# Kernel tuning notes

Hardware: AMD Instinct MI355X
Metric: run time of the kernel (lower is better)

## Reference

```python
import jax, jax.numpy as jnp
import numpy as np

B, S, H = 32, 2048, 1024
UNITS = 1024


def setup_inputs() -> dict:
    key = jax.random.key(0)
    ks = jax.random.split(key, 8)
    scale_h = 1.0 / np.sqrt(H)
    scale_u = 1.0 / np.sqrt(UNITS)
    return {
        "query": jax.random.normal(ks[0], (B, H), dtype=jnp.float32),
        "values": jax.random.normal(ks[1], (B, S, H), dtype=jnp.float32),
        "W1": jax.random.normal(ks[2], (H, UNITS), dtype=jnp.float32) * scale_h,
        "b1": jnp.zeros((UNITS,), dtype=jnp.float32),
        "W2": jax.random.normal(ks[3], (H, UNITS), dtype=jnp.float32) * scale_h,
        "b2": jnp.zeros((UNITS,), dtype=jnp.float32),
        "V": jax.random.normal(ks[4], (UNITS, 1), dtype=jnp.float32) * scale_u,
        "bv": jnp.zeros((1,), dtype=jnp.float32),
    }


def reference(query, values, W1, b1, W2, b2, V, bv):
    # proj_v: [B, S, units]; proj_q: [B, 1, units] (query expanded on time axis)
    proj_v = jnp.einsum("bsh,hu->bsu", values, W1) + b1
    proj_q = (query @ W2 + b2)[:, None, :]
    # score: [B, S, 1]
    score = jnp.tanh(proj_v + proj_q) @ V + bv
    attention_weights = jax.nn.softmax(score, axis=1)  # softmax over seq axis
    context_vector = jnp.sum(attention_weights * values, axis=1)  # [B, H]
    return context_vector, attention_weights
```

## Files before the change

kernel.cpp:

```cpp
#include <hip/hip_runtime.h>

#define H 1024
#define UNITS 1024
#define BATCH 32
#define SEQ 2048
#define M_TOT (BATCH * SEQ)

typedef __attribute__((ext_vector_type(8))) short bf16x8;
typedef __attribute__((ext_vector_type(8))) unsigned short u16x8;
typedef __attribute__((ext_vector_type(4))) float f32x4;

__device__ __forceinline__ unsigned short f2bf(float f) {
  union { float f; unsigned u; } x; x.f = f;
  unsigned r = x.u + 0x7FFFu + ((x.u >> 16) & 1u);
  return (unsigned short)(r >> 16);
}
__device__ __forceinline__ float bf2f(unsigned short h) {
  union { unsigned u; float f; } x; x.u = (unsigned)h << 16;
  return x.f;
}

__device__ __forceinline__ void gll16(const unsigned short* g, unsigned short* l) {
  __builtin_amdgcn_global_load_lds(
      (const __attribute__((address_space(1))) void*)g,
      (__attribute__((address_space(3))) void*)l, 16, 0, 0);
}

__global__ void k_cast(const float* __restrict__ in, unsigned short* __restrict__ out) {
  size_t i = ((size_t)blockIdx.x * 256 + threadIdx.x) * 8;
  float4 v0 = *reinterpret_cast<const float4*>(in + i);
  float4 v1 = *reinterpret_cast<const float4*>(in + i + 4);
  union { unsigned short h[8]; u16x8 v; } p;
  p.h[0] = f2bf(v0.x); p.h[1] = f2bf(v0.y); p.h[2] = f2bf(v0.z); p.h[3] = f2bf(v0.w);
  p.h[4] = f2bf(v1.x); p.h[5] = f2bf(v1.y); p.h[6] = f2bf(v1.z); p.h[7] = f2bf(v1.w);
  *reinterpret_cast<u16x8*>(out + i) = p.v;
}

__global__ void k_transpose_w1(const float* __restrict__ W1, unsigned short* __restrict__ W1T) {
  __shared__ float tile[32][33];
  int bx = blockIdx.x, by = blockIdx.y;
  int tx = threadIdx.x, ty = threadIdx.y;
#pragma unroll
  for (int i = 0; i < 4; ++i)
    tile[ty + i * 8][tx] = W1[(by * 32 + ty + i * 8) * UNITS + bx * 32 + tx];
  __syncthreads();
#pragma unroll
  for (int i = 0; i < 4; ++i)
    W1T[(bx * 32 + ty + i * 8) * H + by * 32 + tx] = f2bf(tile[tx][ty + i * 8]);
}

__global__ void k_projq(const float* __restrict__ query, const float* __restrict__ W2,
                        const float* __restrict__ b2, float* __restrict__ projq) {
  __shared__ float q[H];
  int b = blockIdx.x;
  int u = blockIdx.y * 256 + threadIdx.x;
  for (int i = threadIdx.x; i < H; i += 256) q[i] = query[b * H + i];
  __syncthreads();
  float acc = 0.f;
#pragma unroll 8
  for (int k = 0; k < H; ++k) acc = fmaf(q[k], W2[k * UNITS + u], acc);
  projq[b * UNITS + u] = acc + b2[u];
}

#define BM 256
#define BN 256
#define NKT 32

__global__ __launch_bounds__(512, 2) void k_score3(
    const unsigned short* __restrict__ Vb,
    const unsigned short* __restrict__ W1T,
    const float* __restrict__ b1,
    const float* __restrict__ projq,
    const float* __restrict__ V,
    float* __restrict__ scores)
{
  __shared__ unsigned short As[4][128][64];
  __shared__ unsigned short Bs[4][128][64];

  const int tid = threadIdx.x;
  const int lane = tid & 63;
  const int wave = tid >> 6;
  const int wm = wave >> 2;
  const int wn = wave & 3;
  const int li = lane & 15, hi = lane >> 4;
  const int lr2 = li >> 1;
  const int pcol = (((((li & 1) << 2) + hi) ^ lr2) & 7) << 3;

  const int g = blockIdx.x;
  const int xcd = g & 7;
  const int local = g >> 3;
  const int n_t = local & 3;
  const int m_t = xcd + ((local >> 2) << 3);
  const int m0 = m_t * BM;
  const int n0 = n_t * BN;

  const int sL = (lane & 7) ^ (lane >> 3);
  const int srow = 2 * (lane >> 3) + (sL >> 2);
  const int scol = (sL & 3) << 3;

  auto STAGE_A = [&](int bf, int kt) {
#pragma unroll
    for (int q = 0; q < 2; ++q) {
      int mb = wave * 32 + q * 16;
      gll16(&Vb[(size_t)(m0 + mb + srow) * H + kt * 32 + scol],
            &As[bf][wave * 16 + q * 8][0]);
    }
  };
  auto STAGE_B = [&](int bf, int kt) {
#pragma unroll
    for (int q = 0; q < 2; ++q) {
      int mb = wave * 32 + q * 16;
      gll16(&W1T[(size_t)(n0 + mb + srow) * H + kt * 32 + scol],
            &Bs[bf][wave * 16 + q * 8][0]);
    }
  };

  f32x4 acc[8][4] = {};

  STAGE_A(0, 0); STAGE_B(0, 0);
  STAGE_A(1, 1); STAGE_B(1, 1);
  STAGE_A(2, 2); STAGE_B(2, 2);
  asm volatile("s_waitcnt vmcnt(8)" ::: "memory");
  __builtin_amdgcn_s_barrier();

#pragma unroll 4
  for (int c = 0; c < NKT; ++c) {
    const int buf = c & 3;
    const int nbuf = (c + 3) & 3;
    const int cn = (c < NKT - 3) ? c + 3 : NKT - 1;

    bf16x8 a0[4], a1[4], b[4];

#pragma unroll
    for (int i = 0; i < 4; ++i)
      a0[i] = *reinterpret_cast<const bf16x8*>(&As[buf][wm * 64 + i * 8 + lr2][pcol]);
#pragma unroll
    for (int j = 0; j < 4; ++j)
      b[j] = *reinterpret_cast<const bf16x8*>(&Bs[buf][wn * 32 + j * 8 + lr2][pcol]);
    STAGE_A(nbuf, cn);
    __builtin_amdgcn_s_barrier();
    asm volatile("s_waitcnt lgkmcnt(0)" ::: "memory");
    __builtin_amdgcn_sched_barrier(0);
    __builtin_amdgcn_s_setprio(1);
#pragma unroll
    for (int i = 0; i < 4; ++i)
#pragma unroll
      for (int j = 0; j < 4; ++j)
        acc[i][j] = __builtin_amdgcn_mfma_f32_16x16x32_bf16(a0[i], b[j], acc[i][j], 0, 0, 0);
    __builtin_amdgcn_s_setprio(0);
    __builtin_amdgcn_s_barrier();

#pragma unroll
    for (int i = 0; i < 4; ++i)
      a1[i] = *reinterpret_cast<const bf16x8*>(&As[buf][wm * 64 + (i + 4) * 8 + lr2][pcol]);
    STAGE_B(nbuf, cn);
    asm volatile("s_waitcnt vmcnt(8)" ::: "memory");
    __builtin_amdgcn_s_barrier();
    asm volatile("s_waitcnt lgkmcnt(0)" ::: "memory");
    __builtin_amdgcn_sched_barrier(0);
    __builtin_amdgcn_s_setprio(1);
#pragma unroll
    for (int i = 0; i < 4; ++i)
#pragma unroll
      for (int j = 0; j < 4; ++j)
        acc[i + 4][j] = __builtin_amdgcn_mfma_f32_16x16x32_bf16(a1[i], b[j], acc[i + 4][j], 0, 0, 0);
    __builtin_amdgcn_s_setprio(0);
    __builtin_amdgcn_s_barrier();
  }

  const int b = m0 >> 11;
  float bias[4], vv[4];
#pragma unroll
  for (int j = 0; j < 4; ++j) {
    int u = n0 + wn * 64 + j * 16 + li;
    bias[j] = b1[u] + projq[b * UNITS + u];
    vv[j] = V[u];
  }
#pragma unroll
  for (int mi = 0; mi < 8; ++mi) {
#pragma unroll
    for (int r = 0; r < 4; ++r) {
      float s = 0.f;
#pragma unroll
      for (int j = 0; j < 4; ++j) {
        float x = acc[mi][j][r] + bias[j];
        float e = __expf(2.f * x);
        s += (1.f - 2.f / (e + 1.f)) * vv[j];
      }
      s += __shfl_xor(s, 1);
      s += __shfl_xor(s, 2);
      s += __shfl_xor(s, 4);
      s += __shfl_xor(s, 8);
      if (li == 0) {
        int row = m0 + wm * 128 + mi * 16 + hi * 4 + r;
        atomicAdd(&scores[row], s);
      }
    }
  }
}

#define FBM 128
#define FBN 128
#define FBK 64
#define LDK 72
__global__ __launch_bounds__(256) void k_score_f32(
    const float* __restrict__ values, const unsigned short* __restrict__ W1T,
    const float* __restrict__ b1, const float* __restrict__ projq,
    const float* __restrict__ V, float* __restrict__ scores)
{
  __shared__ unsigned short Asf[FBM][LDK];
  __shared__ unsigned short Bsf[FBN][LDK];
  const int tid = threadIdx.x;
  const int lane = tid & 63;
  const int wave = tid >> 6;
  const int wm = wave >> 1, wn = wave & 1;
  const int li = lane & 15, hi = lane >> 4;
  const int n0 = blockIdx.x * FBN;
  const int m0 = blockIdx.y * FBM;
  f32x4 acc[4][4] = {};
  for (int k0 = 0; k0 < H; k0 += FBK) {
    __syncthreads();
#pragma unroll
    for (int q = 0; q < 8; ++q) {
      int idx = q * 256 + tid;
      int row = idx >> 4;
      int kc = (idx & 15) << 2;
      float4 v = *reinterpret_cast<const float4*>(&values[(size_t)(m0 + row) * H + k0 + kc]);
      union { unsigned short h[4]; unsigned long long u64; } p;
      p.h[0] = f2bf(v.x); p.h[1] = f2bf(v.y); p.h[2] = f2bf(v.z); p.h[3] = f2bf(v.w);
      *reinterpret_cast<unsigned long long*>(&Asf[row][kc]) = p.u64;
    }
#pragma unroll
    for (int q = 0; q < 4; ++q) {
      int idx = q * 256 + tid;
      int row = idx >> 3;
      int kc = (idx & 7) << 3;
      *reinterpret_cast<u16x8*>(&Bsf[row][kc]) =
          *reinterpret_cast<const u16x8*>(&W1T[(size_t)(n0 + row) * H + k0 + kc]);
    }
    __syncthreads();
#pragma unroll
    for (int ks = 0; ks < 2; ++ks) {
      const int kofs = ks * 32 + 8 * hi;
      bf16x8 a[4], bb[4];
#pragma unroll
      for (int i = 0; i < 4; ++i)
        a[i] = *reinterpret_cast<const bf16x8*>(&Asf[wm * 64 + i * 16 + li][kofs]);
#pragma unroll
      for (int i = 0; i < 4; ++i)
        bb[i] = *reinterpret_cast<const bf16x8*>(&Bsf[wn * 64 + i * 16 + li][kofs]);
#pragma unroll
      for (int mi = 0; mi < 4; ++mi)
#pragma unroll
        for (int ni = 0; ni < 4; ++ni)
          acc[mi][ni] = __builtin_amdgcn_mfma_f32_16x16x32_bf16(a[mi], bb[ni], acc[mi][ni], 0, 0, 0);
    }
  }
  const int b = m0 >> 11;
  float bias[4], vv[4];
#pragma unroll
  for (int ni = 0; ni < 4; ++ni) {
    int u = n0 + wn * 64 + ni * 16 + li;
    bias[ni] = b1[u] + projq[b * UNITS + u];
    vv[ni] = V[u];
  }
#pragma unroll
  for (int mi = 0; mi < 4; ++mi) {
#pragma unroll
    for (int r = 0; r < 4; ++r) {
      float s = 0.f;
#pragma unroll
      for (int ni = 0; ni < 4; ++ni) {
        float x = acc[mi][ni][r] + bias[ni];
        float e = __expf(2.f * x);
        s += (1.f - 2.f / (e + 1.f)) * vv[ni];
      }
      s += __shfl_xor(s, 1);
      s += __shfl_xor(s, 2);
      s += __shfl_xor(s, 4);
      s += __shfl_xor(s, 8);
      if (li == 0) atomicAdd(&scores[m0 + wm * 64 + mi * 16 + hi * 4 + r], s);
    }
  }
}

__global__ void k_softmax(const float* __restrict__ scores, float* __restrict__ wts) {
  __shared__ float red[8];
  int b = blockIdx.x;
  int t = threadIdx.x;
  float v[8];
  float mx = -3.4e38f;
#pragma unroll
  for (int i = 0; i < 8; ++i) {
    v[i] = scores[b * SEQ + i * 256 + t];
    mx = fmaxf(mx, v[i]);
  }
#pragma unroll
  for (int o = 1; o < 64; o <<= 1) mx = fmaxf(mx, __shfl_xor(mx, o));
  if ((t & 63) == 0) red[t >> 6] = mx;
  __syncthreads();
  mx = fmaxf(fmaxf(red[0], red[1]), fmaxf(red[2], red[3]));
  float sum = 0.f;
#pragma unroll
  for (int i = 0; i < 8; ++i) { v[i] = __expf(v[i] - mx); sum += v[i]; }
#pragma unroll
  for (int o = 1; o < 64; o <<= 1) sum += __shfl_xor(sum, o);
  if ((t & 63) == 0) red[4 + (t >> 6)] = sum;
  __syncthreads();
  float inv = 1.f / (red[4] + red[5] + red[6] + red[7]);
#pragma unroll
  for (int i = 0; i < 8; ++i) wts[b * SEQ + i * 256 + t] = v[i] * inv;
}

__global__ void k_context_bf(const unsigned short* __restrict__ Vb,
                             const float* __restrict__ wts, float* __restrict__ ctx) {
  int b = blockIdx.x, sc = blockIdx.y;
  int h4 = threadIdx.x * 4;
  const unsigned short* vb = Vb + (size_t)b * SEQ * H;
  float a0 = 0, a1 = 0, a2 = 0, a3 = 0;
  int s0 = sc * 128;
#pragma unroll 4
  for (int s = s0; s < s0 + 128; ++s) {
    float w = wts[b * SEQ + s];
    ushort4 v = *reinterpret_cast<const ushort4*>(&vb[(size_t)s * H + h4]);
    a0 = fmaf(w, bf2f(v.x), a0);
    a1 = fmaf(w, bf2f(v.y), a1);
    a2 = fmaf(w, bf2f(v.z), a2);
    a3 = fmaf(w, bf2f(v.w), a3);
  }
  atomicAdd(&ctx[b * H + h4 + 0], a0);
  atomicAdd(&ctx[b * H + h4 + 1], a1);
  atomicAdd(&ctx[b * H + h4 + 2], a2);
  atomicAdd(&ctx[b * H + h4 + 3], a3);
}

__global__ void k_context(const float* __restrict__ values, const float* __restrict__ wts,
                          float* __restrict__ ctx) {
  int b = blockIdx.x, hc = blockIdx.y, sc = blockIdx.z;
  int h = hc * 256 + threadIdx.x;
  const float* vb = values + (size_t)b * SEQ * H;
  float acc = 0.f;
  int s0 = sc * 128;
#pragma unroll 4
  for (int s = s0; s < s0 + 128; ++s)
    acc = fmaf(wts[b * SEQ + s], vb[(size_t)s * H + h], acc);
  atomicAdd(&ctx[b * H + h], acc);
}

extern "C" void kernel_launch(void* const* d_in, const int* in_sizes, int n_in,
                              void* d_out, int out_size, void* d_ws, size_t ws_size,
                              hipStream_t stream) {
  (void)in_sizes; (void)n_in; (void)out_size;
  const float* query  = (const float*)d_in[0];
  const float* values = (const float*)d_in[1];
  const float* W1     = (const float*)d_in[2];
  const float* b1     = (const float*)d_in[3];
  const float* W2     = (const float*)d_in[4];
  const float* b2     = (const float*)d_in[5];
  const float* V      = (const float*)d_in[6];

  float* out = (float*)d_out;
  float* ctx = out;
  float* wts = out + BATCH * H;

  const size_t vb_bytes = (size_t)M_TOT * H * 2;
  const size_t need = vb_bytes + (2u << 20) + (256u << 10) + (128u << 10);

  if (ws_size >= need) {
    char* ws = (char*)d_ws;
    unsigned short* Vb  = (unsigned short*)ws;
    unsigned short* W1T = (unsigned short*)(ws + vb_bytes);
    float* scores = (float*)(ws + vb_bytes + (2u << 20));
    float* projq  = (float*)(ws + vb_bytes + (2u << 20) + (256u << 10));

    hipMemsetAsync(scores, 0, M_TOT * sizeof(float), stream);
    hipMemsetAsync(ctx, 0, BATCH * H * sizeof(float), stream);

    k_cast<<<(M_TOT * H / 8) / 256, 256, 0, stream>>>(values, Vb);
    k_transpose_w1<<<dim3(32, 32), dim3(32, 8), 0, stream>>>(W1, W1T);
    k_projq<<<dim3(32, 4), 256, 0, stream>>>(query, W2, b2, projq);
    k_score3<<<(M_TOT / BM) * (UNITS / BN), 512, 0, stream>>>(Vb, W1T, b1, projq, V, scores);
    k_softmax<<<BATCH, 256, 0, stream>>>(scores, wts);
    k_context_bf<<<dim3(BATCH, 16), 256, 0, stream>>>(Vb, wts, ctx);
  } else {
    char* ws = (char*)d_ws;
    unsigned short* W1T = (unsigned short*)ws;
    float* scores = (float*)(ws + (2u << 20));
    float* projq  = (float*)(ws + (2u << 20) + (256u << 10));

    hipMemsetAsync(scores, 0, M_TOT * sizeof(float), stream);
    hipMemsetAsync(ctx, 0, BATCH * H * sizeof(float), stream);

    k_transpose_w1<<<dim3(32, 32), dim3(32, 8), 0, stream>>>(W1, W1T);
    k_projq<<<dim3(32, 4), 256, 0, stream>>>(query, W2, b2, projq);
    k_score_f32<<<dim3(UNITS / FBN, M_TOT / FBM), 256, 0, stream>>>(values, W1T, b1, projq, V, scores);
    k_softmax<<<BATCH, 256, 0, stream>>>(scores, wts);
    k_context<<<dim3(BATCH, H / 256, 16), 256, 0, stream>>>(values, wts, ctx);
  }
}
```

Before: 335.3 us.

## Software-pipeline LDS fragment reads with MFMA in GEMM main loop

Restructures the K-loop so the LDS reads for the next half-tile and next tile are issued before the current MFMAs, using double-buffered B fragment registers and partial lgkmcnt waits instead of full lgkmcnt(0) drains. Barriers per tile drop from four to one. The aim is to hide LDS read latency behind matrix work and cut synchronization overhead. It raises register pressure and depends on fine-grained waitcnt counts being correct, so miscounting could cause races.

```diff
diff --git a/kernel.cpp b/kernel.cpp
--- a/kernel.cpp
+++ b/kernel.cpp
@@ -116,57 +116,80 @@
   };
 
   f32x4 acc[8][4] = {};
+  bf16x8 aH0[4], aH1[4], bX[4], bY[4];
+
+  auto READ_H0 = [&](int t, bf16x8* a0, bf16x8* bC) {
+    const int bf = t & 3;
+#pragma unroll
+    for (int i = 0; i < 4; ++i)
+      a0[i] = *reinterpret_cast<const bf16x8*>(&As[bf][wm * 64 + i * 8 + lr2][pcol]);
+#pragma unroll
+    for (int j = 0; j < 4; ++j)
+      bC[j] = *reinterpret_cast<const bf16x8*>(&Bs[bf][wn * 32 + j * 8 + lr2][pcol]);
+  };
+  auto READ_H1 = [&](int t, bf16x8* a1) {
+    const int bf = t & 3;
+#pragma unroll
+    for (int i = 0; i < 4; ++i)
+      a1[i] = *reinterpret_cast<const bf16x8*>(&As[bf][wm * 64 + (i + 4) * 8 + lr2][pcol]);
+  };
+  auto MFMA_H0 = [&](const bf16x8* a0, const bf16x8* bC) {
+    __builtin_amdgcn_s_setprio(1);
+#pragma unroll
+    for (int i = 0; i < 4; ++i)
+#pragma unroll
+      for (int j = 0; j < 4; ++j)
+        acc[i][j] = __builtin_amdgcn_mfma_f32_16x16x32_bf16(a0[i], bC[j], acc[i][j], 0, 0, 0);
+    __builtin_amdgcn_s_setprio(0);
+  };
+  auto MFMA_H1 = [&](const bf16x8* a1, const bf16x8* bC) {
+    __builtin_amdgcn_s_setprio(1);
+#pragma unroll
+    for (int i = 0; i < 4; ++i)
+#pragma unroll
+      for (int j = 0; j < 4; ++j)
+        acc[i + 4][j] = __builtin_amdgcn_mfma_f32_16x16x32_bf16(a1[i], bC[j], acc[i + 4][j], 0, 0, 0);
+    __builtin_amdgcn_s_setprio(0);
+  };
+
+  auto TILE = [&](int tc, bf16x8* bCur, bf16x8* bNxt) {
+    const int cn = (tc + 3 < NKT) ? tc + 3 : NKT - 1;
+    const int nb = (tc + 3) & 3;
+    READ_H1(tc, aH1);
+    STAGE_A(nb, cn);
+    asm volatile("s_waitcnt lgkmcnt(4)" ::: "memory");
+    __builtin_amdgcn_sched_barrier(0);
+    MFMA_H0(aH0, bCur);
+    asm volatile("s_waitcnt vmcnt(6)" ::: "memory");
+    __builtin_amdgcn_s_barrier();
+    READ_H0(tc + 1, aH0, bNxt);
+    STAGE_B(nb, cn);
+    asm volatile("s_waitcnt lgkmcnt(8)" ::: "memory");
+    __builtin_amdgcn_sched_barrier(0);
+    MFMA_H1(aH1, bCur);
+  };
 
   STAGE_A(0, 0); STAGE_B(0, 0);
   STAGE_A(1, 1); STAGE_B(1, 1);
   STAGE_A(2, 2); STAGE_B(2, 2);
   asm volatile("s_waitcnt vmcnt(8)" ::: "memory");
   __builtin_amdgcn_s_barrier();
-
-#pragma unroll 4
-  for (int c = 0; c < NKT; ++c) {
-    const int buf = c & 3;
-    const int nbuf = (c + 3) & 3;
-    const int cn = (c < NKT - 3) ? c + 3 : NKT - 1;
-
-    bf16x8 a0[4], a1[4], b[4];
-
-#pragma unroll
-    for (int i = 0; i < 4; ++i)
-      a0[i] = *reinterpret_cast<const bf16x8*>(&As[buf][wm * 64 + i * 8 + lr2][pcol]);
-#pragma unroll
-    for (int j = 0; j < 4; ++j)
-      b[j] = *reinterpret_cast<const bf16x8*>(&Bs[buf][wn * 32 + j * 8 + lr2][pcol]);
-    STAGE_A(nbuf, cn);
-    __builtin_amdgcn_s_barrier();
-    asm volatile("s_waitcnt lgkmcnt(0)" ::: "memory");
-    __builtin_amdgcn_sched_barrier(0);
-    __builtin_amdgcn_s_setprio(1);
-#pragma unroll
-    for (int i = 0; i < 4; ++i)
-#pragma unroll
-      for (int j = 0; j < 4; ++j)
-        acc[i][j] = __builtin_amdgcn_mfma_f32_16x16x32_bf16(a0[i], b[j], acc[i][j], 0, 0, 0);
-    __builtin_amdgcn_s_setprio(0);
-    __builtin_amdgcn_s_barrier();
-
-#pragma unroll
-    for (int i = 0; i < 4; ++i)
-      a1[i] = *reinterpret_cast<const bf16x8*>(&As[buf][wm * 64 + (i + 4) * 8 + lr2][pcol]);
-    STAGE_B(nbuf, cn);
-    asm volatile("s_waitcnt vmcnt(8)" ::: "memory");
-    __builtin_amdgcn_s_barrier();
-    asm volatile("s_waitcnt lgkmcnt(0)" ::: "memory");
-    __builtin_amdgcn_sched_barrier(0);
-    __builtin_amdgcn_s_setprio(1);
-#pragma unroll
-    for (int i = 0; i < 4; ++i)
-#pragma unroll
-      for (int j = 0; j < 4; ++j)
-        acc[i + 4][j] = __builtin_amdgcn_mfma_f32_16x16x32_bf16(a1[i], b[j], acc[i + 4][j], 0, 0, 0);
-    __builtin_amdgcn_s_setprio(0);
-    __builtin_amdgcn_s_barrier();
-  }
+  READ_H0(0, aH0, bX);
+
+  for (int c = 0; c < NKT - 2; c += 2) {
+    TILE(c, bX, bY);
+    TILE(c + 1, bY, bX);
+  }
+  TILE(NKT - 2, bX, bY);
+  READ_H1(NKT - 1, aH1);
+  asm volatile("s_waitcnt lgkmcnt(4)" ::: "memory");
+  __builtin_amdgcn_sched_barrier(0);
+  MFMA_H0(aH0, bY);
+  asm volatile("s_waitcnt lgkmcnt(0)" ::: "memory");
+  __builtin_amdgcn_sched_barrier(0);
+  MFMA_H1(aH1, bY);
+  asm volatile("s_waitcnt vmcnt(0)" ::: "memory");
+  __builtin_amdgcn_s_barrier();
 
   const int b = m0 >> 11;
   float bias[4], vv[4];
```

New measurement: 336.1 us. Within noise of the previous version (+0.2%).

## Fuse prep kernels and double-buffer LDS fragment reads in score GEMM

Applied to the files above, without the earlier changes.

Merges the bf16 cast, W1 transpose and query projection into one launch so the three small prep kernels share a single dispatch and the small jobs run alongside the cast. It also restructures the score GEMM main loop into a register ping-pong: the LDS reads for the next k-tile go into one register set while MFMAs run on the other, with one barrier pair per tile instead of two half-tile phases. This aims to hide LDS latency behind MFMA and cut barrier count, at the cost of doubling fragment registers, which may reduce occupancy or cause spills at the 2-blocks-per-CU launch bound.

```diff
diff --git a/kernel.cpp b/kernel.cpp
--- a/kernel.cpp
+++ b/kernel.cpp
@@ -26,40 +26,47 @@
       (__attribute__((address_space(3))) void*)l, 16, 0, 0);
 }
 
-__global__ void k_cast(const float* __restrict__ in, unsigned short* __restrict__ out) {
-  size_t i = ((size_t)blockIdx.x * 256 + threadIdx.x) * 8;
-  float4 v0 = *reinterpret_cast<const float4*>(in + i);
-  float4 v1 = *reinterpret_cast<const float4*>(in + i + 4);
-  union { unsigned short h[8]; u16x8 v; } p;
-  p.h[0] = f2bf(v0.x); p.h[1] = f2bf(v0.y); p.h[2] = f2bf(v0.z); p.h[3] = f2bf(v0.w);
-  p.h[4] = f2bf(v1.x); p.h[5] = f2bf(v1.y); p.h[6] = f2bf(v1.z); p.h[7] = f2bf(v1.w);
-  *reinterpret_cast<u16x8*>(out + i) = p.v;
-}
-
-__global__ void k_transpose_w1(const float* __restrict__ W1, unsigned short* __restrict__ W1T) {
-  __shared__ float tile[32][33];
-  int bx = blockIdx.x, by = blockIdx.y;
-  int tx = threadIdx.x, ty = threadIdx.y;
-#pragma unroll
-  for (int i = 0; i < 4; ++i)
-    tile[ty + i * 8][tx] = W1[(by * 32 + ty + i * 8) * UNITS + bx * 32 + tx];
-  __syncthreads();
-#pragma unroll
-  for (int i = 0; i < 4; ++i)
-    W1T[(bx * 32 + ty + i * 8) * H + by * 32 + tx] = f2bf(tile[tx][ty + i * 8]);
-}
-
-__global__ void k_projq(const float* __restrict__ query, const float* __restrict__ W2,
-                        const float* __restrict__ b2, float* __restrict__ projq) {
-  __shared__ float q[H];
-  int b = blockIdx.x;
-  int u = blockIdx.y * 256 + threadIdx.x;
-  for (int i = threadIdx.x; i < H; i += 256) q[i] = query[b * H + i];
-  __syncthreads();
-  float acc = 0.f;
+__global__ void k_prep(const float* __restrict__ values, unsigned short* __restrict__ Vb,
+                       const float* __restrict__ W1, unsigned short* __restrict__ W1T,
+                       const float* __restrict__ query, const float* __restrict__ W2,
+                       const float* __restrict__ b2, float* __restrict__ projq) {
+  __shared__ float sh[1056];
+  const int blk = blockIdx.x;
+  const int tid = threadIdx.x;
+  if (blk < 2048) {
+    for (int u = blk; u < 32768; u += 2048) {
+      size_t i = ((size_t)u * 256 + tid) * 8;
+      float4 v0 = *reinterpret_cast<const float4*>(values + i);
+      float4 v1 = *reinterpret_cast<const float4*>(values + i + 4);
+      union { unsigned short h[8]; u16x8 v; } p;
+      p.h[0] = f2bf(v0.x); p.h[1] = f2bf(v0.y); p.h[2] = f2bf(v0.z); p.h[3] = f2bf(v0.w);
+      p.h[4] = f2bf(v1.x); p.h[5] = f2bf(v1.y); p.h[6] = f2bf(v1.z); p.h[7] = f2bf(v1.w);
+      *reinterpret_cast<u16x8*>(Vb + i) = p.v;
+    }
+  } else if (blk < 3072) {
+    float (*tile)[33] = reinterpret_cast<float(*)[33]>(sh);
+    const int t = blk - 2048;
+    const int bx = t & 31, by = t >> 5;
+    const int tx = tid & 31, ty = tid >> 5;
+#pragma unroll
+    for (int i = 0; i < 4; ++i)
+      tile[ty + i * 8][tx] = W1[(by * 32 + ty + i * 8) * UNITS + bx * 32 + tx];
+    __syncthreads();
+#pragma unroll
+    for (int i = 0; i < 4; ++i)
+      W1T[(bx * 32 + ty + i * 8) * H + by * 32 + tx] = f2bf(tile[tx][ty + i * 8]);
+  } else {
+    float* q = sh;
+    const int t = blk - 3072;
+    const int b = t >> 2;
+    const int u = (t & 3) * 256 + tid;
+    for (int i = tid; i < H; i += 256) q[i] = query[b * H + i];
+    __syncthreads();
+    float acc = 0.f;
 #pragma unroll 8
-  for (int k = 0; k < H; ++k) acc = fmaf(q[k], W2[k * UNITS + u], acc);
-  projq[b * UNITS + u] = acc + b2[u];
+    for (int k = 0; k < H; ++k) acc = fmaf(q[k], W2[k * UNITS + u], acc);
+    projq[b * UNITS + u] = acc + b2[u];
+  }
 }
 
 #define BM 256
@@ -116,57 +123,65 @@
   };
 
   f32x4 acc[8][4] = {};
+  bf16x8 aP[8], bP[4], aQ[8], bQ[4];
+
+  auto READS = [&](int c, bf16x8* rdA, bf16x8* rdB) {
+    const int buf = c & 3;
+#pragma unroll
+    for (int i = 0; i < 8; ++i)
+      rdA[i] = *reinterpret_cast<const bf16x8*>(&As[buf][wm * 64 + i * 8 + lr2][pcol]);
+#pragma unroll
+    for (int j = 0; j < 4; ++j)
+      rdB[j] = *reinterpret_cast<const bf16x8*>(&Bs[buf][wn * 32 + j * 8 + lr2][pcol]);
+  };
+  auto MFMAS = [&](const bf16x8* mA, const bf16x8* mB) {
+    __builtin_amdgcn_s_setprio(1);
+#pragma unroll
+    for (int i = 0; i < 8; ++i)
+#pragma unroll
+      for (int j = 0; j < 4; ++j)
+        acc[i][j] = __builtin_amdgcn_mfma_f32_16x16x32_bf16(mA[i], mB[j], acc[i][j], 0, 0, 0);
+    __builtin_amdgcn_s_setprio(0);
+  };
+  auto BODY = [&](int c, bf16x8* rdA, bf16x8* rdB, const bf16x8* mmA, const bf16x8* mmB) {
+    asm volatile("s_waitcnt vmcnt(8)" ::: "memory");
+    __builtin_amdgcn_s_barrier();
+    READS(c, rdA, rdB);
+    asm volatile("s_waitcnt lgkmcnt(12)" ::: "memory");
+    __builtin_amdgcn_sched_barrier(0);
+    __builtin_amdgcn_s_barrier();
+    const int cn = (c + 3 < NKT) ? c + 3 : NKT - 1;
+    STAGE_A((c + 3) & 3, cn);
+    STAGE_B((c + 3) & 3, cn);
+    __builtin_amdgcn_sched_barrier(0);
+    MFMAS(mmA, mmB);
+  };
 
   STAGE_A(0, 0); STAGE_B(0, 0);
   STAGE_A(1, 1); STAGE_B(1, 1);
   STAGE_A(2, 2); STAGE_B(2, 2);
+
   asm volatile("s_waitcnt vmcnt(8)" ::: "memory");
   __builtin_amdgcn_s_barrier();
-
-#pragma unroll 4
-  for (int c = 0; c < NKT; ++c) {
-    const int buf = c & 3;
-    const int nbuf = (c + 3) & 3;
-    const int cn = (c < NKT - 3) ? c + 3 : NKT - 1;
-
-    bf16x8 a0[4], a1[4], b[4];
-
-#pragma unroll
-    for (int i = 0; i < 4; ++i)
-      a0[i] = *reinterpret_cast<const bf16x8*>(&As[buf][wm * 64 + i * 8 + lr2][pcol]);
-#pragma unroll
-    for (int j = 0; j < 4; ++j)
-      b[j] = *reinterpret_cast<const bf16x8*>(&Bs[buf][wn * 32 + j * 8 + lr2][pcol]);
-    STAGE_A(nbuf, cn);
-    __builtin_amdgcn_s_barrier();
-    asm volatile("s_waitcnt lgkmcnt(0)" ::: "memory");
-    __builtin_amdgcn_sched_barrier(0);
-    __builtin_amdgcn_s_setprio(1);
-#pragma unroll
-    for (int i = 0; i < 4; ++i)
-#pragma unroll
-      for (int j = 0; j < 4; ++j)
-        acc[i][j] = __builtin_amdgcn_mfma_f32_16x16x32_bf16(a0[i], b[j], acc[i][j], 0, 0, 0);
-    __builtin_amdgcn_s_setprio(0);
-    __builtin_amdgcn_s_barrier();
-
-#pragma unroll
-    for (int i = 0; i < 4; ++i)
-      a1[i] = *reinterpret_cast<const bf16x8*>(&As[buf][wm * 64 + (i + 4) * 8 + lr2][pcol]);
-    STAGE_B(nbuf, cn);
-    asm volatile("s_waitcnt vmcnt(8)" ::: "memory");
-    __builtin_amdgcn_s_barrier();
-    asm volatile("s_waitcnt lgkmcnt(0)" ::: "memory");
-    __builtin_amdgcn_sched_barrier(0);
-    __builtin_amdgcn_s_setprio(1);
-#pragma unroll
-    for (int i = 0; i < 4; ++i)
-#pragma unroll
-      for (int j = 0; j < 4; ++j)
-        acc[i + 4][j] = __builtin_amdgcn_mfma_f32_16x16x32_bf16(a1[i], b[j], acc[i + 4][j], 0, 0, 0);
-    __builtin_amdgcn_s_setprio(0);
-    __builtin_amdgcn_s_barrier();
-  }
+  READS(0, aQ, bQ);
+  asm volatile("s_waitcnt lgkmcnt(12)" ::: "memory");
+  __builtin_amdgcn_sched_barrier(0);
+  __builtin_amdgcn_s_barrier();
+  STAGE_A(3, 3);
+  STAGE_B(3, 3);
+  __builtin_amdgcn_sched_barrier(0);
+
+  for (int c = 1; c <= NKT - 3; c += 2) {
+    BODY(c, aP, bP, aQ, bQ);
+    BODY(c + 1, aQ, bQ, aP, bP);
+  }
+  BODY(NKT - 1, aP, bP, aQ, bQ);
+
+  asm volatile("s_waitcnt lgkmcnt(0)" ::: "memory");
+  __builtin_amdgcn_sched_barrier(0);
+  MFMAS(aP, bP);
+  asm volatile("s_waitcnt vmcnt(0)" ::: "memory");
+  __builtin_amdgcn_s_barrier();
 
   const int b = m0 >> 11;
   float bias[4], vv[4];
@@ -197,6 +212,32 @@
       }
     }
   }
+}
+
+__global__ void k_transpose_w1(const float* __restrict__ W1, unsigned short* __restrict__ W1T) {
+  __shared__ float tile[32][33];
+  int bx = blockIdx.x, by = blockIdx.y;
+  int tx = threadIdx.x, ty = threadIdx.y;
+#pragma unroll
+  for (int i = 0; i < 4; ++i)
+    tile[ty + i * 8][tx] = W1[(by * 32 + ty + i * 8) * UNITS + bx * 32 + tx];
+  __syncthreads();
+#pragma unroll
+  for (int i = 0; i < 4; ++i)
+    W1T[(bx * 32 + ty + i * 8) * H + by * 32 + tx] = f2bf(tile[tx][ty + i * 8]);
+}
+
+__global__ void k_projq(const float* __restrict__ query, const float* __restrict__ W2,
+                        const float* __restrict__ b2, float* __restrict__ projq) {
+  __shared__ float q[H];
+  int b = blockIdx.x;
+  int u = blockIdx.y * 256 + threadIdx.x;
+  for (int i = threadIdx.x; i < H; i += 256) q[i] = query[b * H + i];
+  __syncthreads();
+  float acc = 0.f;
+#pragma unroll 8
+  for (int k = 0; k < H; ++k) acc = fmaf(q[k], W2[k * UNITS + u], acc);
+  projq[b * UNITS + u] = acc + b2[u];
 }
 
 #define FBM 128
@@ -376,9 +417,7 @@
     hipMemsetAsync(scores, 0, M_TOT * sizeof(float), stream);
     hipMemsetAsync(ctx, 0, BATCH * H * sizeof(float), stream);
 
-    k_cast<<<(M_TOT * H / 8) / 256, 256, 0, stream>>>(values, Vb);
-    k_transpose_w1<<<dim3(32, 32), dim3(32, 8), 0, stream>>>(W1, W1T);
-    k_projq<<<dim3(32, 4), 256, 0, stream>>>(query, W2, b2, projq);
+    k_prep<<<3200, 256, 0, stream>>>(values, Vb, W1, W1T, query, W2, b2, projq);
     k_score3<<<(M_TOT / BM) * (UNITS / BN), 512, 0, stream>>>(Vb, W1T, b1, projq, V, scores);
     k_softmax<<<BATCH, 256, 0, stream>>>(scores, wts);
     k_context_bf<<<dim3(BATCH, 16), 256, 0, stream>>>(Vb, wts, ctx);
```

After: 329.7 us. About the same (-1.7%).
